# Optimization experiments

Measured on AMD Instinct MI355X. Metric: run time of the kernel, lower is better.

## Reference

```python
import jax, jax.numpy as jnp
import numpy as np


def _patches3x3(x):
    # x: [B,H,W,C] -> [B,H,W,9,C], SAME zero padding, patch index k = i*3+j
    B, H, W, C = x.shape
    p = jnp.pad(x, ((0, 0), (1, 1), (1, 1), (0, 0)))
    return jnp.stack([p[:, i:i + H, j:j + W, :] for i in range(3) for j in range(3)], axis=3)


def setup_inputs() -> dict:
    key = jax.random.key(0)
    k1, k2, k3 = jax.random.split(key, 3)
    B, H, W, CH, NC, DIM = 4, 80, 80, 256, 22, 256
    x = jax.random.normal(k1, (B, H, W, CH), dtype=jnp.float32)
    seg_mask = jax.random.uniform(k2, (B, H, W, NC), dtype=jnp.float32)
    # he_uniform over receptive field ch*3*3
    lim = np.sqrt(6.0 / (CH * 9)).astype(np.float32)
    conv_w = jax.random.uniform(k3, (CH, 3, 3, DIM), dtype=jnp.float32, minval=-lim, maxval=lim)
    return {"x": x, "seg_mask": seg_mask, "conv_w": conv_w}


def reference(x, seg_mask, conv_w):
    B, H, W, CH = x.shape
    NC = seg_mask.shape[-1]
    DIM = conv_w.shape[-1]
    # patches of segmentation map: [B,H,W,9,NC]
    s_patch = _patches3x3(seg_mask)
    m = seg_mask[:, :, :, None, :]                       # [B,H,W,1,NC]
    s_max = jnp.max(m, axis=-1, keepdims=True)           # [B,H,W,1,1]
    # keep patch values only for the argmax class at the center pixel
    sel = jnp.sum(jnp.where(m == s_max, s_patch, 0.0), axis=-1)  # [B,H,W,9]
    cnt = jnp.sum((sel != 0.0).astype(jnp.float32), axis=-1, keepdims=True)  # [B,H,W,1]
    norm = jnp.where(cnt > 0, 9.0 / jnp.maximum(cnt, 1.0), 0.0)  # divide_no_nan(9, cnt)
    # per-channel 3x3 patch extraction of features (== depthwise conv with eye(9))
    xp = _patches3x3(x)                                  # [B,H,W,9,CH]
    xp = xp * sel[..., None]                             # mask-gated patches
    w = conv_w.reshape(CH, 9, DIM)
    out = jnp.einsum('bhwkc,ckd->bhwd', xp, w) * norm    # [B,H,W,DIM]
    return out
```

## Files before the change

kernel.cpp:

```cpp
#include <hip/hip_runtime.h>
#include <hip/hip_bf16.h>
#include <cstdint>

#define B_ 4
#define H_ 80
#define W_ 80
#define CH_ 256
#define NC_ 22
#define DIM_ 256
#define NPIX (B_*H_*W_)

typedef unsigned short ushort;
typedef __attribute__((ext_vector_type(8))) short short8;
typedef __attribute__((ext_vector_type(4))) float floatx4;

static __device__ inline ushort f2bf(float v) {
    __hip_bfloat16 h = __float2bfloat16(v);
    ushort r;
    __builtin_memcpy(&r, &h, 2);
    return r;
}
static __device__ inline unsigned pk2(float a, float b) {
    return (unsigned)f2bf(a) | ((unsigned)f2bf(b) << 16);
}

__global__ __launch_bounds__(256) void prep(const float* __restrict__ seg,
                                            const float* __restrict__ cw,
                                            const float* __restrict__ x,
                                            float* __restrict__ ssel,
                                            ushort* __restrict__ wbT,
                                            ushort* __restrict__ xb)
{
    __shared__ ushort ls[32][260];
    if (blockIdx.x < 900) {
        const int t = blockIdx.x * 256 + threadIdx.x;
        const int k = t / NPIX;
        const int m = t - k * NPIX;
        const int w = m % W_;
        const int h = (m / W_) % H_;
        const int b = m / (W_ * H_);

        const float2* c2 = (const float2*)(seg + (size_t)m * NC_);
        float cv[NC_];
        #pragma unroll
        for (int c = 0; c < NC_ / 2; ++c) { float2 v = c2[c]; cv[2*c] = v.x; cv[2*c+1] = v.y; }
        float mx = -1e30f;
        #pragma unroll
        for (int c = 0; c < NC_; ++c) mx = fmaxf(mx, cv[c]);

        const int i = k / 3, j = k % 3;
        const int hh = h + i - 1, ww = w + j - 1;
        float s = 0.f;
        if (hh >= 0 && hh < H_ && ww >= 0 && ww < W_) {
            const float2* n2 = (const float2*)(seg + ((size_t)((b * H_ + hh) * W_ + ww)) * NC_);
            #pragma unroll
            for (int c = 0; c < NC_ / 2; ++c) {
                float2 v = n2[c];
                s += (cv[2*c]   == mx) ? v.x : 0.f;
                s += (cv[2*c+1] == mx) ? v.y : 0.f;
            }
        }
        ssel[t] = s;
    } else if (blockIdx.x < 972) {
        const int bx = blockIdx.x - 900;
        const int k  = bx / 8;
        const int c0 = (bx % 8) * 32;
        const int c    = threadIdx.x >> 3;
        const int seg8 = threadIdx.x & 7;

        const float* src = cw + ((size_t)(c0 + c) * 9 + k) * DIM_ + seg8 * 32;
        #pragma unroll
        for (int e = 0; e < 32; e += 4) {
            float4 v = *(const float4*)(src + e);
            unsigned* dst = (unsigned*)&ls[c][seg8 * 32 + e];
            dst[0] = pk2(v.x, v.y);
            dst[1] = pk2(v.z, v.w);
        }
        __syncthreads();

        const int d = threadIdx.x;
        ushort tmp[32];
        #pragma unroll
        for (int cc = 0; cc < 32; ++cc) tmp[cc] = ls[cc][d];
        uint4 o[4];
        __builtin_memcpy(o, tmp, 64);
        uint4* dst = (uint4*)(wbT + ((size_t)k * 256 + d) * 256 + c0);
        dst[0] = o[0]; dst[1] = o[1]; dst[2] = o[2]; dst[3] = o[3];
    } else if (xb != nullptr) {
        size_t idx = ((size_t)(blockIdx.x - 972) * 256 + threadIdx.x) * 8;
        const float4* s = (const float4*)(x + idx);
        float4 a = s[0], b = s[1];
        uint4 o = make_uint4(pk2(a.x, a.y), pk2(a.z, a.w), pk2(b.x, b.y), pk2(b.z, b.w));
        *(uint4*)(xb + idx) = o;
    }
}

template<bool XB16>
__global__ __launch_bounds__(256, 3) void conv2(const float* __restrict__ x,
                                                const ushort* __restrict__ xb,
                                                const float* __restrict__ ssel,
                                                const ushort* __restrict__ wbT,
                                                float* __restrict__ out)
{
    __shared__ ushort xsA[2][80 * 136];
    __shared__ float  sl[9][80];

    const int tid  = threadIdx.x;
    const int lane = tid & 63;
    const int wv   = tid >> 6;
    const int ln   = lane & 15;
    const int quad = lane >> 4;
    const int rt   = blockIdx.x;
    const int b    = rt / H_;
    const int h    = rt % H_;
    const int d0   = blockIdx.y * 128;

    int qm[5], qc[5];
    #pragma unroll
    for (int r = 0; r < 5; ++r) {
        int q = tid + 256 * r;
        qm[r] = q >> 4;
        qc[r] = q & 15;
    }

    floatx4 O[5][2];
    #pragma unroll
    for (int i = 0; i < 5; ++i)
        #pragma unroll
        for (int jn = 0; jn < 2; ++jn)
            O[i][jn] = (floatx4){0.f, 0.f, 0.f, 0.f};

    uint4  sg[5];
    float4 fa[5], fb[5];
    bool   ok[5];

    auto stage_load = [&](int nit) {
        const int i   = nit / 6;
        const int rem = nit % 6;
        const int cc  = (rem / 3) * 128;
        const int jj  = rem % 3;
        const int rr  = h + i - 1;
        const bool rowok = (rr >= 0) && (rr < H_);
        const int rsafe = rowok ? rr : h;
        #pragma unroll
        for (int r = 0; r < 5; ++r) {
            const int col = qm[r] + jj - 1;
            const bool v = rowok && (col >= 0) && (col < W_);
            ok[r] = v;
            const size_t gp = ((size_t)(b * H_ + rsafe) * W_ + (v ? col : 0));
            if (XB16) {
                sg[r] = *(const uint4*)(xb + gp * CH_ + cc + qc[r] * 8);
            } else {
                const float* f = x + gp * CH_ + cc + qc[r] * 8;
                fa[r] = *(const float4*)f;
                fb[r] = *(const float4*)(f + 4);
            }
        }
    };
    auto stage_write = [&](int nit) {
        ushort* bp = xsA[nit & 1];
        #pragma unroll
        for (int r = 0; r < 5; ++r) {
            uint4 v;
            if (XB16) {
                v = ok[r] ? sg[r] : make_uint4(0u, 0u, 0u, 0u);
            } else {
                v = ok[r] ? make_uint4(pk2(fa[r].x, fa[r].y), pk2(fa[r].z, fa[r].w),
                                       pk2(fb[r].x, fb[r].y), pk2(fb[r].z, fb[r].w))
                          : make_uint4(0u, 0u, 0u, 0u);
            }
            *(uint4*)&bp[qm[r] * 136 + qc[r] * 8] = v;
        }
    };

    short8 Breg[8];
    auto loadB = [&](int nit) {
        const int i   = nit / 6;
        const int rem = nit % 6;
        const int cc  = (rem / 3) * 128;
        const int jj  = rem % 3;
        const int k   = 3 * i + jj;
        #pragma unroll
        for (int kk = 0; kk < 4; ++kk)
            #pragma unroll
            for (int jn = 0; jn < 2; ++jn)
                Breg[kk * 2 + jn] = *(const short8*)(wbT
                    + ((size_t)k * 256 + d0 + wv * 32 + jn * 16 + ln) * 256
                    + cc + kk * 32 + quad * 8);
    };

    stage_load(0);
    if (tid < 80) {
        float rv[9]; int cnt = 0;
        #pragma unroll
        for (int k = 0; k < 9; ++k) {
            rv[k] = ssel[k * NPIX + rt * W_ + tid];
            cnt += (rv[k] != 0.f) ? 1 : 0;
        }
        const float norm = (cnt > 0) ? 9.f / (float)cnt : 0.f;
        #pragma unroll
        for (int k = 0; k < 9; ++k) sl[k][tid] = rv[k] * norm;
    }
    stage_write(0);
    loadB(0);
    __syncthreads();

    #pragma unroll 2
    for (int it = 0; it < 18; ++it) {
        const int i   = it / 6;
        const int rem = it % 6;
        const int jj  = rem % 3;
        const int k   = 3 * i + jj;
        const ushort* bp = xsA[it & 1];

        if (it < 17) stage_load(it + 1);

        floatx4 P[5][2];
        #pragma unroll
        for (int im = 0; im < 5; ++im)
            #pragma unroll
            for (int jn = 0; jn < 2; ++jn)
                P[im][jn] = (floatx4){0.f, 0.f, 0.f, 0.f};

        #pragma unroll
        for (int kk = 0; kk < 4; ++kk) {
            short8 a[5];
            #pragma unroll
            for (int im = 0; im < 5; ++im)
                a[im] = *(const short8*)&bp[(im * 16 + ln) * 136 + kk * 32 + quad * 8];
            #pragma unroll
            for (int im = 0; im < 5; ++im)
                #pragma unroll
                for (int jn = 0; jn < 2; ++jn)
                    P[im][jn] = __builtin_amdgcn_mfma_f32_16x16x32_bf16(
                        a[im], Breg[kk * 2 + jn], P[im][jn], 0, 0, 0);
        }

        if (it < 17) stage_write(it + 1);
        if (it < 17) loadB(it + 1);

        #pragma unroll
        for (int im = 0; im < 5; ++im) {
            const float4 sv = *(const float4*)&sl[k][im * 16 + quad * 4];
            #pragma unroll
            for (int jn = 0; jn < 2; ++jn) {
                O[im][jn][0] += sv.x * P[im][jn][0];
                O[im][jn][1] += sv.y * P[im][jn][1];
                O[im][jn][2] += sv.z * P[im][jn][2];
                O[im][jn][3] += sv.w * P[im][jn][3];
            }
        }
        __syncthreads();
    }

    #pragma unroll
    for (int im = 0; im < 5; ++im) {
        #pragma unroll
        for (int jn = 0; jn < 2; ++jn) {
            const int dd = d0 + wv * 32 + jn * 16 + ln;
            #pragma unroll
            for (int r = 0; r < 4; ++r) {
                const int m = im * 16 + quad * 4 + r;
                out[((size_t)(rt * W_ + m)) * DIM_ + dd] = O[im][jn][r];
            }
        }
    }
}

extern "C" void kernel_launch(void* const* d_in, const int* in_sizes, int n_in,
                              void* d_out, int out_size, void* d_ws, size_t ws_size,
                              hipStream_t stream)
{
    const float* x   = (const float*)d_in[0];
    const float* seg = (const float*)d_in[1];
    const float* cw  = (const float*)d_in[2];
    float* out = (float*)d_out;

    float*  ssel = (float*)d_ws;
    ushort* wbT  = (ushort*)((char*)d_ws + 921600);
    ushort* xb   = (ushort*)((char*)d_ws + 921600 + 1179648);
    const size_t need = 921600u + 1179648u + 13107200u;

    if (ws_size >= need) {
        prep<<<dim3(972 + 3200), dim3(256), 0, stream>>>(seg, cw, x, ssel, wbT, xb);
        conv2<true><<<dim3(B_ * H_, 2), dim3(256), 0, stream>>>(x, xb, ssel, wbT, out);
    } else {
        prep<<<dim3(972), dim3(256), 0, stream>>>(seg, cw, x, ssel, wbT, nullptr);
        conv2<false><<<dim3(B_ * H_, 2), dim3(256), 0, stream>>>(x, nullptr, ssel, wbT, out);
    }
}
```

Measured before the change: 156.4 us.

## Stage bf16 activation tiles via direct global-to-LDS loads with XOR swizzle

Replaces the register-staged load/convert/store of activation tiles in the bf16 path with global_load_lds 16-byte transfers straight into LDS. Out-of-bounds pixels point at a static zero buffer. The padded 136-stride layout becomes a 128-stride layout with an XOR swizzle to avoid bank conflicts. This is meant to cut VGPR pressure and VALU/LDS-store instructions in the staging path, at the cost of depending on correct async-LDS ordering under the existing barrier. The fp32 fallback is split into a separate unchanged kernel.

```diff
diff --git a/kernel.cpp b/kernel.cpp
--- a/kernel.cpp
+++ b/kernel.cpp
@@ -14,6 +14,8 @@
 typedef __attribute__((ext_vector_type(8))) short short8;
 typedef __attribute__((ext_vector_type(4))) float floatx4;
 
+__device__ __attribute__((aligned(256))) static const unsigned char zglob[256] = {};
+
 static __device__ inline ushort f2bf(float v) {
     __hip_bfloat16 h = __float2bfloat16(v);
     ushort r;
@@ -22,6 +24,10 @@
 }
 static __device__ inline unsigned pk2(float a, float b) {
     return (unsigned)f2bf(a) | ((unsigned)f2bf(b) << 16);
+}
+static __device__ inline void gll16(const void* g, void* l) {
+    __builtin_amdgcn_global_load_lds((const __attribute__((address_space(1))) void*)g,
+                                     (__attribute__((address_space(3))) void*)l, 16, 0, 0);
 }
 
 __global__ __launch_bounds__(256) void prep(const float* __restrict__ seg,
@@ -95,15 +101,13 @@
     }
 }
 
-template<bool XB16>
-__global__ __launch_bounds__(256, 3) void conv2(const float* __restrict__ x,
-                                                const ushort* __restrict__ xb,
+__global__ __launch_bounds__(256, 3) void conv2(const ushort* __restrict__ xb,
                                                 const float* __restrict__ ssel,
                                                 const ushort* __restrict__ wbT,
                                                 float* __restrict__ out)
 {
-    __shared__ ushort xsA[2][80 * 136];
-    __shared__ float  sl[9][80];
+    __shared__ __attribute__((aligned(1024))) ushort xs[2][80 * 128];
+    __shared__ float sl[9][80];
 
     const int tid  = threadIdx.x;
     const int lane = tid & 63;
@@ -115,63 +119,12 @@
     const int h    = rt % H_;
     const int d0   = blockIdx.y * 128;
 
-    int qm[5], qc[5];
-    #pragma unroll
-    for (int r = 0; r < 5; ++r) {
-        int q = tid + 256 * r;
-        qm[r] = q >> 4;
-        qc[r] = q & 15;
-    }
-
     floatx4 O[5][2];
     #pragma unroll
     for (int i = 0; i < 5; ++i)
         #pragma unroll
         for (int jn = 0; jn < 2; ++jn)
             O[i][jn] = (floatx4){0.f, 0.f, 0.f, 0.f};
-
-    uint4  sg[5];
-    float4 fa[5], fb[5];
-    bool   ok[5];
-
-    auto stage_load = [&](int nit) {
-        const int i   = nit / 6;
-        const int rem = nit % 6;
-        const int cc  = (rem / 3) * 128;
-        const int jj  = rem % 3;
-        const int rr  = h + i - 1;
-        const bool rowok = (rr >= 0) && (rr < H_);
-        const int rsafe = rowok ? rr : h;
-        #pragma unroll
-        for (int r = 0; r < 5; ++r) {
-            const int col = qm[r] + jj - 1;
-            const bool v = rowok && (col >= 0) && (col < W_);
-            ok[r] = v;
-            const size_t gp = ((size_t)(b * H_ + rsafe) * W_ + (v ? col : 0));
-            if (XB16) {
-                sg[r] = *(const uint4*)(xb + gp * CH_ + cc + qc[r] * 8);
-            } else {
-                const float* f = x + gp * CH_ + cc + qc[r] * 8;
-                fa[r] = *(const float4*)f;
-                fb[r] = *(const float4*)(f + 4);
-            }
-        }
-    };
-    auto stage_write = [&](int nit) {
-        ushort* bp = xsA[nit & 1];
-        #pragma unroll
-        for (int r = 0; r < 5; ++r) {
-            uint4 v;
-            if (XB16) {
-                v = ok[r] ? sg[r] : make_uint4(0u, 0u, 0u, 0u);
-            } else {
-                v = ok[r] ? make_uint4(pk2(fa[r].x, fa[r].y), pk2(fa[r].z, fa[r].w),
-                                       pk2(fb[r].x, fb[r].y), pk2(fb[r].z, fb[r].w))
-                          : make_uint4(0u, 0u, 0u, 0u);
-            }
-            *(uint4*)&bp[qm[r] * 136 + qc[r] * 8] = v;
-        }
-    };
 
     short8 Breg[8];
     auto loadB = [&](int nit) {
@@ -189,7 +142,31 @@
                     + cc + kk * 32 + quad * 8);
     };
 
-    stage_load(0);
+    auto stage = [&](int nit) {
+        const int i   = nit / 6;
+        const int rem = nit % 6;
+        const int cc  = (rem / 3) * 128;
+        const int jj  = rem % 3;
+        const int rr  = h + i - 1;
+        const bool rowok = (rr >= 0) && (rr < H_);
+        const ushort* xrow = xb + ((size_t)((b * H_ + (rowok ? rr : 0)) * W_)) * CH_ + cc;
+        char* dbase = (char*)&xs[nit & 1][0];
+        #pragma unroll
+        for (int r = 0; r < 5; ++r) {
+            const int s    = (r * 4 + wv) * 64 + lane;
+            const int p    = s >> 4;
+            const int cph  = s & 15;
+            const int clog = cph ^ (p & 7);
+            const int col  = p + jj - 1;
+            const bool v   = rowok && (col >= 0) && (col < W_);
+            const void* src = v ? (const void*)(xrow + (size_t)col * CH_ + clog * 8)
+                                : (const void*)zglob;
+            gll16(src, dbase + (size_t)(r * 4 + wv) * 1024);
+        }
+    };
+
+    stage(0);
+    loadB(0);
     if (tid < 80) {
         float rv[9]; int cnt = 0;
         #pragma unroll
@@ -201,8 +178,6 @@
         #pragma unroll
         for (int k = 0; k < 9; ++k) sl[k][tid] = rv[k] * norm;
     }
-    stage_write(0);
-    loadB(0);
     __syncthreads();
 
     #pragma unroll 2
@@ -211,9 +186,9 @@
         const int rem = it % 6;
         const int jj  = rem % 3;
         const int k   = 3 * i + jj;
-        const ushort* bp = xsA[it & 1];
-
-        if (it < 17) stage_load(it + 1);
+        const char* bp = (const char*)&xs[it & 1][0];
+
+        if (it < 17) stage(it + 1);
 
         floatx4 P[5][2];
         #pragma unroll
@@ -227,7 +202,9 @@
             short8 a[5];
             #pragma unroll
             for (int im = 0; im < 5; ++im)
-                a[im] = *(const short8*)&bp[(im * 16 + ln) * 136 + kk * 32 + quad * 8];
+                a[im] = *(const short8*)(bp
+                    + (size_t)(im * 16 + ln) * 256
+                    + ((((kk << 2) | quad) ^ (ln & 7)) << 4));
             #pragma unroll
             for (int im = 0; im < 5; ++im)
                 #pragma unroll
@@ -236,7 +213,6 @@
                         a[im], Breg[kk * 2 + jn], P[im][jn], 0, 0, 0);
         }
 
-        if (it < 17) stage_write(it + 1);
         if (it < 17) loadB(it + 1);
 
         #pragma unroll
@@ -265,6 +241,149 @@
             }
         }
     }
+}
+
+__global__ __launch_bounds__(256, 3) void conv2_fb(const float* __restrict__ x,
+                                                   const float* __restrict__ ssel,
+                                                   const ushort* __restrict__ wbT,
+                                                   float* __restrict__ out)
+{
+    __shared__ ushort xsA[2][80 * 136];
+    __shared__ float  sl[9][80];
+
+    const int tid  = threadIdx.x;
+    const int lane = tid & 63;
+    const int wv   = tid >> 6;
+    const int ln   = lane & 15;
+    const int quad = lane >> 4;
+    const int rt   = blockIdx.x;
+    const int b    = rt / H_;
+    const int h    = rt % H_;
+    const int d0   = blockIdx.y * 128;
+
+    int qm[5], qc[5];
+    #pragma unroll
+    for (int r = 0; r < 5; ++r) { int q = tid + 256 * r; qm[r] = q >> 4; qc[r] = q & 15; }
+
+    floatx4 O[5][2];
+    #pragma unroll
+    for (int i = 0; i < 5; ++i)
+        #pragma unroll
+        for (int jn = 0; jn < 2; ++jn)
+            O[i][jn] = (floatx4){0.f, 0.f, 0.f, 0.f};
+
+    float4 fa[5], fb[5];
+    bool   ok[5];
+
+    auto stage_load = [&](int nit) {
+        const int i = nit / 6, rem = nit % 6, cc = (rem / 3) * 128, jj = rem % 3;
+        const int rr = h + i - 1;
+        const bool rowok = (rr >= 0) && (rr < H_);
+        const int rsafe = rowok ? rr : h;
+        #pragma unroll
+        for (int r = 0; r < 5; ++r) {
+            const int col = qm[r] + jj - 1;
+            const bool v = rowok && (col >= 0) && (col < W_);
+            ok[r] = v;
+            const float* f = x + ((size_t)(b * H_ + rsafe) * W_ + (v ? col : 0)) * CH_ + cc + qc[r] * 8;
+            fa[r] = *(const float4*)f;
+            fb[r] = *(const float4*)(f + 4);
+        }
+    };
+    auto stage_write = [&](int nit) {
+        ushort* bp = xsA[nit & 1];
+        #pragma unroll
+        for (int r = 0; r < 5; ++r) {
+            uint4 v = ok[r] ? make_uint4(pk2(fa[r].x, fa[r].y), pk2(fa[r].z, fa[r].w),
+                                         pk2(fb[r].x, fb[r].y), pk2(fb[r].z, fb[r].w))
+                            : make_uint4(0u, 0u, 0u, 0u);
+            *(uint4*)&bp[qm[r] * 136 + qc[r] * 8] = v;
+        }
+    };
+
+    short8 Breg[8];
+    auto loadB = [&](int nit) {
+        const int i = nit / 6, rem = nit % 6, cc = (rem / 3) * 128, jj = rem % 3;
+        const int k = 3 * i + jj;
+        #pragma unroll
+        for (int kk = 0; kk < 4; ++kk)
+            #pragma unroll
+            for (int jn = 0; jn < 2; ++jn)
+                Breg[kk * 2 + jn] = *(const short8*)(wbT
+                    + ((size_t)k * 256 + d0 + wv * 32 + jn * 16 + ln) * 256
+                    + cc + kk * 32 + quad * 8);
+    };
+
+    stage_load(0);
+    if (tid < 80) {
+        float rv[9]; int cnt = 0;
+        #pragma unroll
+        for (int k = 0; k < 9; ++k) { rv[k] = ssel[k * NPIX + rt * W_ + tid]; cnt += (rv[k] != 0.f) ? 1 : 0; }
+        const float norm = (cnt > 0) ? 9.f / (float)cnt : 0.f;
+        #pragma unroll
+        for (int k = 0; k < 9; ++k) sl[k][tid] = rv[k] * norm;
+    }
+    stage_write(0);
+    loadB(0);
+    __syncthreads();
+
+    #pragma unroll 2
+    for (int it = 0; it < 18; ++it) {
+        const int i = it / 6, rem = it % 6, jj = rem % 3;
+        const int k = 3 * i + jj;
+        const ushort* bp = xsA[it & 1];
+
+        if (it < 17) stage_load(it + 1);
+
+        floatx4 P[5][2];
+        #pragma unroll
+        for (int im = 0; im < 5; ++im)
+            #pragma unroll
+            for (int jn = 0; jn < 2; ++jn)
+                P[im][jn] = (floatx4){0.f, 0.f, 0.f, 0.f};
+
+        #pragma unroll
+        for (int kk = 0; kk < 4; ++kk) {
+            short8 a[5];
+            #pragma unroll
+            for (int im = 0; im < 5; ++im)
+                a[im] = *(const short8*)&bp[(im * 16 + ln) * 136 + kk * 32 + quad * 8];
+            #pragma unroll
+            for (int im = 0; im < 5; ++im)
+                #pragma unroll
+                for (int jn = 0; jn < 2; ++jn)
+                    P[im][jn] = __builtin_amdgcn_mfma_f32_16x16x32_bf16(
+                        a[im], Breg[kk * 2 + jn], P[im][jn], 0, 0, 0);
+        }
+
+        if (it < 17) stage_write(it + 1);
+        if (it < 17) loadB(it + 1);
+
+        #pragma unroll
+        for (int im = 0; im < 5; ++im) {
+            const float4 sv = *(const float4*)&sl[k][im * 16 + quad * 4];
+            #pragma unroll
+            for (int jn = 0; jn < 2; ++jn) {
+                O[im][jn][0] += sv.x * P[im][jn][0];
+                O[im][jn][1] += sv.y * P[im][jn][1];
+                O[im][jn][2] += sv.z * P[im][jn][2];
+                O[im][jn][3] += sv.w * P[im][jn][3];
+            }
+        }
+        __syncthreads();
+    }
+
+    #pragma unroll
+    for (int im = 0; im < 5; ++im)
+        #pragma unroll
+        for (int jn = 0; jn < 2; ++jn) {
+            const int dd = d0 + wv * 32 + jn * 16 + ln;
+            #pragma unroll
+            for (int r = 0; r < 4; ++r) {
+                const int m = im * 16 + quad * 4 + r;
+                out[((size_t)(rt * W_ + m)) * DIM_ + dd] = O[im][jn][r];
+            }
+        }
 }
 
 extern "C" void kernel_launch(void* const* d_in, const int* in_sizes, int n_in,
@@ -283,9 +402,9 @@
 
     if (ws_size >= need) {
         prep<<<dim3(972 + 3200), dim3(256), 0, stream>>>(seg, cw, x, ssel, wbT, xb);
-        conv2<true><<<dim3(B_ * H_, 2), dim3(256), 0, stream>>>(x, xb, ssel, wbT, out);
+        conv2<<<dim3(B_ * H_, 2), dim3(256), 0, stream>>>(xb, ssel, wbT, out);
     } else {
         prep<<<dim3(972), dim3(256), 0, stream>>>(seg, cw, x, ssel, wbT, nullptr);
-        conv2<false><<<dim3(B_ * H_, 2), dim3(256), 0, stream>>>(x, nullptr, ssel, wbT, out);
-    }
-}
+        conv2_fb<<<dim3(B_ * H_, 2), dim3(256), 0, stream>>>(x, ssel, wbT, out);
+    }
+}
```

Measured after the change: 149.4 us. 4.5% less time.
